# Kernel optimization log

Measured on AMD Instinct MI355X. Metric: run time of the kernel, lower is better.

## Reference

```python
import jax, jax.numpy as jnp
import numpy as np

N_NODES = 50000
N_EDGES = 500000
HIDDEN = 128
HEADS = 8
HEAD_DIM = HIDDEN // HEADS


def setup_inputs() -> dict:
    key = jax.random.key(0)
    ks = jax.random.split(key, 20)

    def lin_w(k, fin, fout):
        return (jax.random.normal(k, (fin, fout), jnp.float32) / np.sqrt(fin)).astype(jnp.float32)

    inp = {
        "h": jax.random.normal(ks[0], (N_NODES, HIDDEN), jnp.float32),
        "x": jax.random.normal(ks[1], (N_NODES, 3), jnp.float32),
        "src": jax.random.randint(ks[2], (N_EDGES,), 0, N_NODES, jnp.int32),
        "dst": jax.random.randint(ks[3], (N_EDGES,), 0, N_NODES, jnp.int32),
        "distances": jax.random.uniform(ks[4], (N_EDGES,), jnp.float32),
        # linear layers stored as [in, out] (transposed vs torch nn.Linear)
        "Wq": lin_w(ks[5], HIDDEN, HIDDEN), "bq": jnp.zeros((HIDDEN,), jnp.float32),
        "Wk": lin_w(ks[6], HIDDEN, HIDDEN), "bk": jnp.zeros((HIDDEN,), jnp.float32),
        "Wv": lin_w(ks[7], HIDDEN, HIDDEN), "bv": jnp.zeros((HIDDEN,), jnp.float32),
        "Wo": lin_w(ks[8], HIDDEN, HIDDEN), "bo": jnp.zeros((HIDDEN,), jnp.float32),
        "Wd": lin_w(ks[9], 1, HEADS), "bd": jnp.zeros((HEADS,), jnp.float32),
        "Wg1": lin_w(ks[10], HIDDEN, HIDDEN), "bg1": jnp.zeros((HIDDEN,), jnp.float32),
        "Wg2": lin_w(ks[11], HIDDEN, 1), "bg2": jnp.zeros((1,), jnp.float32),
    }
    return inp


def reference(h, x, src, dst, distances,
              Wq, bq, Wk, bk, Wv, bv, Wo, bo, Wd, bd, Wg1, bg1, Wg2, bg2):
    n = h.shape[0]
    heads = Wd.shape[1]
    dh = Wq.shape[1] // heads

    q = (h @ Wq + bq).reshape(n, heads, dh)
    k = (h @ Wk + bk).reshape(n, heads, dh)
    v = (h @ Wv + bv).reshape(n, heads, dh)

    q_src = q[src]            # [E, heads, dh]
    k_dst = k[dst]
    v_dst = v[dst]

    logits = jnp.einsum('ehd,ehd->eh', q_src, k_dst) / jnp.sqrt(jnp.asarray(dh, h.dtype))
    bias = (distances * distances)[:, None] @ Wd + bd      # [E, heads]
    lg = logits - bias

    # segment softmax over edges grouped by src node
    m = jax.ops.segment_max(lg, src, num_segments=n)        # [N, heads]
    ex = jnp.exp(lg - m[src])
    s = jax.ops.segment_sum(ex, src, num_segments=n)
    w = ex / jnp.maximum(s[src], 1e-9)                      # [E, heads]

    h_upd = jax.ops.segment_sum(v_dst * w[:, :, None], src, num_segments=n)
    h_out = h + h_upd.reshape(n, heads * dh) @ Wo + bo

    w_mean = w.mean(axis=1)                                 # mean over heads -> [E]
    disp = jax.ops.segment_sum((x[dst] - x[src]) * w_mean[:, None], src, num_segments=n)

    gate = jnp.tanh(jax.nn.silu(h_out @ Wg1 + bg1) @ Wg2 + bg2)  # [N, 1]
    x_out = x + gate * disp
    return (h_out, x_out)
```

## Files before the change

### kernel.cpp

```cpp
#include <hip/hip_runtime.h>
#include <math.h>

#define N_NODES 50000
#define N_EDGES 500000
#define HIDDEN 128
#define HEADS 8
#define HEAD_DIM 16

#define QB 391
#define QKV_TOTAL 782
#define SCAT_BLOCKS 1954
#define SPLITW_BLOCKS 320
#define ZERO_BLOCKS 196
#define NSCANB 49

typedef __attribute__((ext_vector_type(8))) short short8;
typedef __attribute__((ext_vector_type(4))) float floatx4;

#define OFF_Q       0u
#define OFF_KV      6400000u
#define OFF_HHI     12800000u
#define OFF_HLO     16000000u
#define OFF_DISP    19200000u
#define OFF_CNT     19350016u
#define OFF_ROWPTR  19400032u
#define OFF_CURSOR  19450048u
#define OFF_ESD     19500064u
#define OFF_WSPLIT  20500064u

static __device__ __forceinline__ unsigned short f2bf(float f) {
    unsigned u = __builtin_bit_cast(unsigned, f);
    unsigned r = (u + 0x7FFFu + ((u >> 16) & 1u)) >> 16;
    return (unsigned short)r;
}
static __device__ __forceinline__ float bf2f(unsigned short s) {
    return __builtin_bit_cast(float, (unsigned)s << 16);
}

__global__ void k_prep(const float* __restrict__ Wq, const float* __restrict__ Wk,
                       const float* __restrict__ Wv, const float* __restrict__ Wo,
                       const float* __restrict__ Wg1, unsigned short* __restrict__ ws,
                       int* __restrict__ cnt, int* __restrict__ flag) {
    if (blockIdx.x >= SPLITW_BLOCKS) {
        int i = (int)(blockIdx.x - SPLITW_BLOCKS) * 256 + threadIdx.x;
        if (i < N_NODES) cnt[i] = 0;
        if (i < 64) flag[i] = 0;
        return;
    }
    int t = blockIdx.x * 256 + threadIdx.x;
    int m = t >> 14, r = t & 16383;
    int k = r >> 7, n = r & 127;
    const float* W = (m == 0) ? Wq : (m == 1) ? Wk : (m == 2) ? Wv : (m == 3) ? Wo : Wg1;
    float x = W[k * 128 + n];
    int kc = k >> 5, kin = k & 31, quad = kin >> 3, j = kin & 7;
    int ct = n >> 4, nin = n & 15, lane = quad * 16 + nin;
    unsigned base = ((((unsigned)(m * 4 + kc) * 8 + ct) * 2) * 64 + lane) * 8 + j;
    unsigned short a = f2bf(x);
    ws[base] = a;
    ws[base + 512] = f2bf(x - bf2f(a));
}

__global__ void k_count(const int* __restrict__ src, int* __restrict__ cnt,
                        int* __restrict__ rnk) {
    int e = blockIdx.x * 256 + threadIdx.x;
    if (e < N_EDGES) rnk[e] = atomicAdd(&cnt[src[e]], 1);
}

__global__ __launch_bounds__(1024) void k_scan(const int* __restrict__ cnt,
                                               int* __restrict__ rowptr,
                                               int* __restrict__ agg,
                                               int* __restrict__ flag) {
    __shared__ int buf[1024];
    __shared__ int sh_off;
    const int b = blockIdx.x, t = threadIdx.x;
    const int i = b * 1024 + t;
    int val = (i < N_NODES) ? cnt[i] : 0;
    buf[t] = val;
    __syncthreads();
    for (int off = 1; off < 1024; off <<= 1) {
        int a = (t >= off) ? buf[t - off] : 0;
        __syncthreads();
        buf[t] += a;
        __syncthreads();
    }
    if (t == 1023) {
        agg[b] = buf[1023];
        __threadfence();
        atomicExch(&flag[b], 1);
    }
    if (t < 64) {
        int s = 0;
        if (t < b) {
            while (atomicAdd(&flag[t], 0) == 0) { }
            __threadfence();
            s = agg[t];
        }
#pragma unroll
        for (int off = 1; off < 64; off <<= 1) s += __shfl_xor(s, off);
        if (t == 0) sh_off = s;
    }
    __syncthreads();
    const int exoff = sh_off;
    if (i < N_NODES) rowptr[i + 1] = buf[t] + exoff;
    if (i == 0) rowptr[0] = 0;
}

__global__ __launch_bounds__(256, 2) void k_qkv_scatter(
    const float* __restrict__ h, const unsigned short* __restrict__ wsp,
    const float* __restrict__ bq, const float* __restrict__ bk, const float* __restrict__ bv,
    float* __restrict__ q, unsigned* __restrict__ kvp,
    const int* __restrict__ src, const int* __restrict__ dst,
    const float* __restrict__ dist, const int* __restrict__ rowptr,
    const int* __restrict__ rnk, int2* __restrict__ esd) {
    if (blockIdx.x >= QKV_TOTAL) {
        int e = (int)(blockIdx.x - QKV_TOTAL) * 256 + threadIdx.x;
        if (e < N_EDGES) {
            int s = src[e];
            float dd = dist[e];
            int pos = rowptr[s] + rnk[e];
            esd[pos] = make_int2(dst[e], __float_as_int(dd * dd));
        }
        return;
    }

    __shared__ short lds[32768];
    const int tid = threadIdx.x;
    const int wave = tid >> 6, lane = tid & 63;
    const int quad = lane >> 4, l15 = lane & 15;
    const bool iskv = (blockIdx.x >= QB);
    const int blk = iskv ? (int)blockIdx.x - QB : (int)blockIdx.x;
    const int row0 = blk * 128 + wave * 32;

    short8 ah[2][4], al[2][4];
#pragma unroll
    for (int rt = 0; rt < 2; ++rt) {
        int row = row0 + rt * 16 + l15;
        if (row >= N_NODES) row = N_NODES - 1;
        const float* hp = h + (size_t)row * 128;
#pragma unroll
        for (int kc = 0; kc < 4; ++kc) {
            const float* p = hp + kc * 32 + quad * 8;
            float4 f0 = *(const float4*)(p);
            float4 f1 = *(const float4*)(p + 4);
            float fv[8] = {f0.x, f0.y, f0.z, f0.w, f1.x, f1.y, f1.z, f1.w};
#pragma unroll
            for (int j = 0; j < 8; ++j) {
                unsigned short hi = f2bf(fv[j]);
                ah[rt][kc][j] = (short)hi;
                al[rt][kc][j] = (short)f2bf(fv[j] - bf2f(hi));
            }
        }
    }

    auto stage = [&](int m) {
        const float4* s4 = (const float4*)(wsp + (unsigned)m * 32768u);
        float4* d4 = (float4*)lds;
#pragma unroll 4
        for (int it = tid; it < 4096; it += 256) d4[it] = s4[it];
    };

    auto compute = [&](floatx4 (&acc)[2][8]) {
#pragma unroll
        for (int kc = 0; kc < 4; ++kc) {
#pragma unroll
            for (int ct = 0; ct < 8; ++ct) {
                const short* tb = lds + (((kc * 8 + ct) * 2) * 64 + lane) * 8;
                short8 bh = *(const short8*)(tb);
                short8 bl = *(const short8*)(tb + 512);
#pragma unroll
                for (int rt = 0; rt < 2; ++rt) {
                    acc[rt][ct] = __builtin_amdgcn_mfma_f32_16x16x32_bf16(
                        ah[rt][kc], bh, acc[rt][ct], 0, 0, 0);
                    acc[rt][ct] = __builtin_amdgcn_mfma_f32_16x16x32_bf16(
                        ah[rt][kc], bl, acc[rt][ct], 0, 0, 0);
                    acc[rt][ct] = __builtin_amdgcn_mfma_f32_16x16x32_bf16(
                        al[rt][kc], bh, acc[rt][ct], 0, 0, 0);
                }
            }
        }
    };

    if (!iskv) {
        stage(0);
        __syncthreads();
        floatx4 acc[2][8];
#pragma unroll
        for (int rt = 0; rt < 2; ++rt)
#pragma unroll
            for (int ct = 0; ct < 8; ++ct) acc[rt][ct] = (floatx4){0.f, 0.f, 0.f, 0.f};
        compute(acc);
#pragma unroll
        for (int ct = 0; ct < 8; ++ct) {
            int col = ct * 16 + l15;
            float b = bq[col];
#pragma unroll
            for (int rt = 0; rt < 2; ++rt)
#pragma unroll
                for (int reg = 0; reg < 4; ++reg) {
                    int row = row0 + rt * 16 + quad * 4 + reg;
                    if (row < N_NODES) q[(size_t)row * 128 + col] = acc[rt][ct][reg] + b;
                }
        }
    } else {
        stage(1);
        __syncthreads();
        floatx4 acc[2][8];
#pragma unroll
        for (int rt = 0; rt < 2; ++rt)
#pragma unroll
            for (int ct = 0; ct < 8; ++ct) acc[rt][ct] = (floatx4){0.f, 0.f, 0.f, 0.f};
        compute(acc);
        unsigned kb[2][8][2];
#pragma unroll
        for (int ct = 0; ct < 8; ++ct) {
            float b = bk[ct * 16 + l15];
#pragma unroll
            for (int rt = 0; rt < 2; ++rt) {
                kb[rt][ct][0] = (unsigned)f2bf(acc[rt][ct][0] + b) |
                                ((unsigned)f2bf(acc[rt][ct][1] + b) << 16);
                kb[rt][ct][1] = (unsigned)f2bf(acc[rt][ct][2] + b) |
                                ((unsigned)f2bf(acc[rt][ct][3] + b) << 16);
            }
        }
        __syncthreads();
        stage(2);
        __syncthreads();
#pragma unroll
        for (int rt = 0; rt < 2; ++rt)
#pragma unroll
            for (int ct = 0; ct < 8; ++ct) acc[rt][ct] = (floatx4){0.f, 0.f, 0.f, 0.f};
        compute(acc);
#pragma unroll
        for (int ct = 0; ct < 8; ++ct) {
            int col = ct * 16 + l15;
            float b = bv[col];
#pragma unroll
            for (int rt = 0; rt < 2; ++rt)
#pragma unroll
                for (int reg = 0; reg < 4; ++reg) {
                    int row = row0 + rt * 16 + quad * 4 + reg;
                    unsigned vb = f2bf(acc[rt][ct][reg] + b);
                    unsigned kw = (kb[rt][ct][reg >> 1] >> ((reg & 1) * 16)) & 0xFFFFu;
                    if (row < N_NODES) kvp[(size_t)row * 128 + col] = kw | (vb << 16);
                }
        }
    }
}

__global__ __launch_bounds__(256) void k_edge_node(
    const float* __restrict__ q, const unsigned* __restrict__ kvp,
    const float* __restrict__ x,
    const int2* __restrict__ esd, const int* __restrict__ rowptr,
    const float* __restrict__ Wd, const float* __restrict__ bd,
    unsigned short* __restrict__ hupd_hi, unsigned short* __restrict__ hupd_lo,
    float* __restrict__ disp) {
    const int wave = threadIdx.x >> 6, lane = threadIdx.x & 63;
    const int node = blockIdx.x * 4 + wave;
    const int h = lane >> 3, sub = lane & 7;
    const int beg = rowptr[node], end = rowptr[node + 1];

    float2 qv = *(const float2*)(q + (size_t)node * 128 + 2 * lane);
    qv.x *= 0.25f; qv.y *= 0.25f;
    const float wdh = Wd[h];
    const bool dal = (sub < 3);
    float xs = dal ? x[node * 3 + sub] : 0.f;
    const unsigned colo = 2 * lane;

    float acc0 = 0.f, acc1 = 0.f, s_own = 0.f, da = 0.f;

    for (int cb = beg; cb < end; cb += 4) {
        int2 ed[4]; uint2 kv2[4]; float xg[4]; float msk[4];
#pragma unroll
        for (int j = 0; j < 4; ++j) {
            int idx = cb + j;
            msk[j] = (idx < end) ? 1.f : 0.f;
            if (idx >= end) idx = end - 1;
            ed[j] = esd[idx];
        }
#pragma unroll
        for (int j = 0; j < 4; ++j)
            kv2[j] = *(const uint2*)(kvp + (unsigned)ed[j].x * 128u + colo);
#pragma unroll
        for (int j = 0; j < 4; ++j)
            xg[j] = dal ? x[(unsigned)ed[j].x * 3u + sub] : 0.f;
#pragma unroll
        for (int j = 0; j < 4; ++j) {
            float k0 = __builtin_bit_cast(float, kv2[j].x << 16);
            float v0 = __builtin_bit_cast(float, kv2[j].x & 0xFFFF0000u);
            float k1 = __builtin_bit_cast(float, kv2[j].y << 16);
            float v1 = __builtin_bit_cast(float, kv2[j].y & 0xFFFF0000u);
            float p = qv.x * k0 + qv.y * k1;
            p += __shfl_xor(p, 1);
            p += __shfl_xor(p, 2);
            p += __shfl_xor(p, 4);
            float w = __expf(p - __int_as_float(ed[j].y) * wdh) * msk[j];
            s_own += w;
            acc0 += v0 * w;
            acc1 += v1 * w;
            da += (xg[j] - xs) * w;
        }
    }

    float inva = 1.f / fmaxf(s_own, 1e-9f);
    float o0 = acc0 * inva, o1 = acc1 * inva;
    unsigned short h0 = f2bf(o0), h1 = f2bf(o1);
    unsigned short l0 = f2bf(o0 - bf2f(h0)), l1 = f2bf(o1 - bf2f(h1));
    ((unsigned*)hupd_hi)[(size_t)node * 64 + lane] = (unsigned)h0 | ((unsigned)h1 << 16);
    ((unsigned*)hupd_lo)[(size_t)node * 64 + lane] = (unsigned)l0 | ((unsigned)l1 << 16);

    da *= 0.125f * inva;
    da += __shfl_xor(da, 8);
    da += __shfl_xor(da, 16);
    da += __shfl_xor(da, 32);
    if (lane < 3) disp[node * 3 + lane] = da;
}

__global__ __launch_bounds__(256) void k_hout_gate(
    const float* __restrict__ h,
    const unsigned short* __restrict__ hupd_hi, const unsigned short* __restrict__ hupd_lo,
    const unsigned short* __restrict__ wsp,
    const float* __restrict__ bo, const float* __restrict__ bg1,
    const float* __restrict__ Wg2, const float* __restrict__ bg2,
    const float* __restrict__ x, const float* __restrict__ disp,
    float* __restrict__ hout, float* __restrict__ xout) {
    __shared__ float hb[4][16 * 132];
    const int wave = threadIdx.x >> 6, lane = threadIdx.x & 63;
    const int quad = lane >> 4, l15 = lane & 15;
    const int row0 = blockIdx.x * 64 + wave * 16;
    float* hbw = hb[wave];

    floatx4 acc[8];
#pragma unroll
    for (int c = 0; c < 8; ++c) acc[c] = (floatx4){0.f, 0.f, 0.f, 0.f};
#pragma unroll
    for (int kc = 0; kc < 4; ++kc) {
        int row = row0 + l15;
        if (row >= N_NODES) row = N_NODES - 1;
        size_t aoff = (size_t)row * 128 + kc * 32 + quad * 8;
        short8 ah = *(const short8*)(hupd_hi + aoff);
        short8 al = *(const short8*)(hupd_lo + aoff);
#pragma unroll
        for (int ct = 0; ct < 8; ++ct) {
            unsigned fb = ((((unsigned)(3 * 4 + kc) * 8 + ct) * 2) * 64 + lane) * 8;
            short8 bh = *(const short8*)(wsp + fb);
            short8 bl = *(const short8*)(wsp + fb + 512);
            acc[ct] = __builtin_amdgcn_mfma_f32_16x16x32_bf16(ah, bh, acc[ct], 0, 0, 0);
            acc[ct] = __builtin_amdgcn_mfma_f32_16x16x32_bf16(ah, bl, acc[ct], 0, 0, 0);
            acc[ct] = __builtin_amdgcn_mfma_f32_16x16x32_bf16(al, bh, acc[ct], 0, 0, 0);
        }
    }

#pragma unroll
    for (int ct = 0; ct < 8; ++ct) {
        int col = ct * 16 + l15;
        float bias = bo[col];
#pragma unroll
        for (int reg = 0; reg < 4; ++reg) {
            int row = row0 + quad * 4 + reg;
            float val = acc[ct][reg] + bias;
            if (row < N_NODES) {
                val += h[(size_t)row * 128 + col];
                hout[(size_t)row * 128 + col] = val;
            }
            hbw[(quad * 4 + reg) * 132 + col] = val;
        }
    }
    __asm__ volatile("s_waitcnt lgkmcnt(0)" ::: "memory");

    floatx4 acc2[8];
#pragma unroll
    for (int c = 0; c < 8; ++c) acc2[c] = (floatx4){0.f, 0.f, 0.f, 0.f};
#pragma unroll
    for (int kc = 0; kc < 4; ++kc) {
        const float* ap = hbw + l15 * 132 + kc * 32 + quad * 8;
        float4 f0 = *(const float4*)(ap);
        float4 f1 = *(const float4*)(ap + 4);
        float fv[8] = {f0.x, f0.y, f0.z, f0.w, f1.x, f1.y, f1.z, f1.w};
        short8 ah, al;
#pragma unroll
        for (int j = 0; j < 8; ++j) {
            unsigned short hi = f2bf(fv[j]);
            ah[j] = (short)hi;
            al[j] = (short)f2bf(fv[j] - bf2f(hi));
        }
#pragma unroll
        for (int ct = 0; ct < 8; ++ct) {
            unsigned fb = ((((unsigned)(4 * 4 + kc) * 8 + ct) * 2) * 64 + lane) * 8;
            short8 bh = *(const short8*)(wsp + fb);
            short8 bl = *(const short8*)(wsp + fb + 512);
            acc2[ct] = __builtin_amdgcn_mfma_f32_16x16x32_bf16(ah, bh, acc2[ct], 0, 0, 0);
            acc2[ct] = __builtin_amdgcn_mfma_f32_16x16x32_bf16(ah, bl, acc2[ct], 0, 0, 0);
            acc2[ct] = __builtin_amdgcn_mfma_f32_16x16x32_bf16(al, bh, acc2[ct], 0, 0, 0);
        }
    }

    float pr[4] = {0.f, 0.f, 0.f, 0.f};
#pragma unroll
    for (int ct = 0; ct < 8; ++ct) {
        int col = ct * 16 + l15;
        float b1 = bg1[col];
        float w2 = Wg2[col];
#pragma unroll
        for (int reg = 0; reg < 4; ++reg) {
            float z = acc2[ct][reg] + b1;
            pr[reg] += (z / (1.f + __expf(-z))) * w2;
        }
    }
#pragma unroll
    for (int off = 1; off < 16; off <<= 1) {
#pragma unroll
        for (int reg = 0; reg < 4; ++reg) pr[reg] += __shfl_xor(pr[reg], off);
    }
    if (l15 == 0) {
        float b2 = bg2[0];
#pragma unroll
        for (int reg = 0; reg < 4; ++reg) {
            int row = row0 + quad * 4 + reg;
            if (row < N_NODES) {
                float g = tanhf(pr[reg] + b2);
#pragma unroll
                for (int dd = 0; dd < 3; ++dd) {
                    int oo = row * 3 + dd;
                    xout[oo] = x[oo] + g * disp[oo];
                }
            }
        }
    }
}

extern "C" void kernel_launch(void* const* d_in, const int* in_sizes, int n_in,
                              void* d_out, int out_size, void* d_ws, size_t ws_size,
                              hipStream_t stream) {
    const float* h    = (const float*)d_in[0];
    const float* x    = (const float*)d_in[1];
    const int*   src  = (const int*)d_in[2];
    const int*   dst  = (const int*)d_in[3];
    const float* dist = (const float*)d_in[4];
    const float* Wq = (const float*)d_in[5];  const float* bq = (const float*)d_in[6];
    const float* Wk = (const float*)d_in[7];  const float* bk = (const float*)d_in[8];
    const float* Wv = (const float*)d_in[9];  const float* bv = (const float*)d_in[10];
    const float* Wo = (const float*)d_in[11]; const float* bo = (const float*)d_in[12];
    const float* Wd = (const float*)d_in[13]; const float* bd = (const float*)d_in[14];
    const float* Wg1 = (const float*)d_in[15]; const float* bg1 = (const float*)d_in[16];
    const float* Wg2 = (const float*)d_in[17]; const float* bg2 = (const float*)d_in[18];

    float* ws    = (float*)d_ws;
    float* q     = ws + OFF_Q;
    unsigned* kvp = (unsigned*)(ws + OFF_KV);
    float* disp  = ws + OFF_DISP;
    int* cnt     = (int*)(ws + OFF_CNT);
    int* rowptr  = (int*)(ws + OFF_ROWPTR);
    int* agg     = (int*)(ws + OFF_CURSOR);
    int* flag    = agg + 64;
    int2* esd    = (int2*)(ws + OFF_ESD);
    unsigned short* wsp = (unsigned short*)(ws + OFF_WSPLIT);
    int* rank   = (int*)(ws + OFF_HHI);
    unsigned short* hupd_hi = (unsigned short*)(ws + OFF_HHI);
    unsigned short* hupd_lo = (unsigned short*)(ws + OFF_HLO);
    float* hout = (float*)d_out;
    float* xout = hout + (size_t)N_NODES * HIDDEN;

    k_prep<<<SPLITW_BLOCKS + ZERO_BLOCKS, 256, 0, stream>>>(Wq, Wk, Wv, Wo, Wg1, wsp,
                                                            cnt, flag);
    k_count<<<SCAT_BLOCKS, 256, 0, stream>>>(src, cnt, rank);
    k_scan<<<NSCANB, 1024, 0, stream>>>(cnt, rowptr, agg, flag);
    k_qkv_scatter<<<QKV_TOTAL + SCAT_BLOCKS, 256, 0, stream>>>(
        h, wsp, bq, bk, bv, q, kvp, src, dst, dist, rowptr, rank, esd);
    k_edge_node<<<N_NODES / 4, 256, 0, stream>>>(q, kvp, x, esd, rowptr,
                                                 Wd, bd, hupd_hi, hupd_lo, disp);
    k_hout_gate<<<(N_NODES + 63) / 64, 256, 0, stream>>>(h, hupd_hi, hupd_lo, wsp,
                                                         bo, bg1, Wg2, bg2,
                                                         x, disp, hout, xout);
}
```

Measured before the change: 265.4 us.

## Batch edge-index loads via wave shuffles and double row tiles in hout/gate GEMM

```diff
diff --git a/kernel.cpp b/kernel.cpp
--- a/kernel.cpp
+++ b/kernel.cpp
@@ -13,6 +13,7 @@
 #define SPLITW_BLOCKS 320
 #define ZERO_BLOCKS 196
 #define NSCANB 49
+#define HG_BLOCKS 391
 
 typedef __attribute__((ext_vector_type(8))) short short8;
 typedef __attribute__((ext_vector_type(4))) float floatx4;
@@ -268,36 +269,64 @@
 
     float acc0 = 0.f, acc1 = 0.f, s_own = 0.f, da = 0.f;
 
-    for (int cb = beg; cb < end; cb += 4) {
-        int2 ed[4]; uint2 kv2[4]; float xg[4]; float msk[4];
-#pragma unroll
-        for (int j = 0; j < 4; ++j) {
-            int idx = cb + j;
-            msk[j] = (idx < end) ? 1.f : 0.f;
-            if (idx >= end) idx = end - 1;
-            ed[j] = esd[idx];
-        }
-#pragma unroll
-        for (int j = 0; j < 4; ++j)
-            kv2[j] = *(const uint2*)(kvp + (unsigned)ed[j].x * 128u + colo);
-#pragma unroll
-        for (int j = 0; j < 4; ++j)
-            xg[j] = dal ? x[(unsigned)ed[j].x * 3u + sub] : 0.f;
-#pragma unroll
-        for (int j = 0; j < 4; ++j) {
-            float k0 = __builtin_bit_cast(float, kv2[j].x << 16);
-            float v0 = __builtin_bit_cast(float, kv2[j].x & 0xFFFF0000u);
-            float k1 = __builtin_bit_cast(float, kv2[j].y << 16);
-            float v1 = __builtin_bit_cast(float, kv2[j].y & 0xFFFF0000u);
+    for (int cb = beg; cb < end; cb += 64) {
+        int idx = cb + lane;
+        int dvec = 0; float d2vec = 0.f;
+        if (idx < end) {
+            int2 ed = esd[idx];
+            dvec = ed.x;
+            d2vec = __int_as_float(ed.y);
+        }
+        int clen = min(64, end - cb);
+        int i = 0;
+        for (; i + 4 <= clen; i += 4) {
+            int di[4]; float dd2[4]; uint2 kv2[4]; float xg[4];
+#pragma unroll
+            for (int j = 0; j < 4; ++j) {
+                di[j]  = __shfl(dvec, i + j);
+                dd2[j] = __shfl(d2vec, i + j);
+            }
+#pragma unroll
+            for (int j = 0; j < 4; ++j)
+                kv2[j] = *(const uint2*)(kvp + (unsigned)di[j] * 128u + colo);
+#pragma unroll
+            for (int j = 0; j < 4; ++j)
+                xg[j] = dal ? x[(unsigned)di[j] * 3u + sub] : 0.f;
+#pragma unroll
+            for (int j = 0; j < 4; ++j) {
+                float k0 = __builtin_bit_cast(float, kv2[j].x << 16);
+                float v0 = __builtin_bit_cast(float, kv2[j].x & 0xFFFF0000u);
+                float k1 = __builtin_bit_cast(float, kv2[j].y << 16);
+                float v1 = __builtin_bit_cast(float, kv2[j].y & 0xFFFF0000u);
+                float p = qv.x * k0 + qv.y * k1;
+                p += __shfl_xor(p, 1);
+                p += __shfl_xor(p, 2);
+                p += __shfl_xor(p, 4);
+                float w = __expf(p - dd2[j] * wdh);
+                s_own += w;
+                acc0 += v0 * w;
+                acc1 += v1 * w;
+                da += (xg[j] - xs) * w;
+            }
+        }
+        for (; i < clen; ++i) {
+            int dij  = __shfl(dvec, i);
+            float d2 = __shfl(d2vec, i);
+            uint2 kv2 = *(const uint2*)(kvp + (unsigned)dij * 128u + colo);
+            float xgj = dal ? x[(unsigned)dij * 3u + sub] : 0.f;
+            float k0 = __builtin_bit_cast(float, kv2.x << 16);
+            float v0 = __builtin_bit_cast(float, kv2.x & 0xFFFF0000u);
+            float k1 = __builtin_bit_cast(float, kv2.y << 16);
+            float v1 = __builtin_bit_cast(float, kv2.y & 0xFFFF0000u);
             float p = qv.x * k0 + qv.y * k1;
             p += __shfl_xor(p, 1);
             p += __shfl_xor(p, 2);
             p += __shfl_xor(p, 4);
-            float w = __expf(p - __int_as_float(ed[j].y) * wdh) * msk[j];
+            float w = __expf(p - d2 * wdh);
             s_own += w;
             acc0 += v0 * w;
             acc1 += v1 * w;
-            da += (xg[j] - xs) * w;
+            da += (xgj - xs) * w;
         }
     }
 
@@ -315,7 +344,7 @@
     if (lane < 3) disp[node * 3 + lane] = da;
 }
 
-__global__ __launch_bounds__(256) void k_hout_gate(
+__global__ __launch_bounds__(256, 2) void k_hout_gate(
     const float* __restrict__ h,
     const unsigned short* __restrict__ hupd_hi, const unsigned short* __restrict__ hupd_lo,
     const unsigned short* __restrict__ wsp,
@@ -323,30 +352,39 @@
     const float* __restrict__ Wg2, const float* __restrict__ bg2,
     const float* __restrict__ x, const float* __restrict__ disp,
     float* __restrict__ hout, float* __restrict__ xout) {
-    __shared__ float hb[4][16 * 132];
+    __shared__ float hb[4][32 * 132];
     const int wave = threadIdx.x >> 6, lane = threadIdx.x & 63;
     const int quad = lane >> 4, l15 = lane & 15;
-    const int row0 = blockIdx.x * 64 + wave * 16;
+    const int row0 = blockIdx.x * 128 + wave * 32;
     float* hbw = hb[wave];
 
-    floatx4 acc[8];
-#pragma unroll
-    for (int c = 0; c < 8; ++c) acc[c] = (floatx4){0.f, 0.f, 0.f, 0.f};
+    floatx4 acc[2][8];
+#pragma unroll
+    for (int rt = 0; rt < 2; ++rt)
+#pragma unroll
+        for (int c = 0; c < 8; ++c) acc[rt][c] = (floatx4){0.f, 0.f, 0.f, 0.f};
 #pragma unroll
     for (int kc = 0; kc < 4; ++kc) {
-        int row = row0 + l15;
-        if (row >= N_NODES) row = N_NODES - 1;
-        size_t aoff = (size_t)row * 128 + kc * 32 + quad * 8;
-        short8 ah = *(const short8*)(hupd_hi + aoff);
-        short8 al = *(const short8*)(hupd_lo + aoff);
+        short8 ah[2], al[2];
+#pragma unroll
+        for (int rt = 0; rt < 2; ++rt) {
+            int row = row0 + rt * 16 + l15;
+            if (row >= N_NODES) row = N_NODES - 1;
+            size_t aoff = (size_t)row * 128 + kc * 32 + quad * 8;
+            ah[rt] = *(const short8*)(hupd_hi + aoff);
+            al[rt] = *(const short8*)(hupd_lo + aoff);
+        }
 #pragma unroll
         for (int ct = 0; ct < 8; ++ct) {
             unsigned fb = ((((unsigned)(3 * 4 + kc) * 8 + ct) * 2) * 64 + lane) * 8;
             short8 bh = *(const short8*)(wsp + fb);
             short8 bl = *(const short8*)(wsp + fb + 512);
-            acc[ct] = __builtin_amdgcn_mfma_f32_16x16x32_bf16(ah, bh, acc[ct], 0, 0, 0);
-            acc[ct] = __builtin_amdgcn_mfma_f32_16x16x32_bf16(ah, bl, acc[ct], 0, 0, 0);
-            acc[ct] = __builtin_amdgcn_mfma_f32_16x16x32_bf16(al, bh, acc[ct], 0, 0, 0);
+#pragma unroll
+            for (int rt = 0; rt < 2; ++rt) {
+                acc[rt][ct] = __builtin_amdgcn_mfma_f32_16x16x32_bf16(ah[rt], bh, acc[rt][ct], 0, 0, 0);
+                acc[rt][ct] = __builtin_amdgcn_mfma_f32_16x16x32_bf16(ah[rt], bl, acc[rt][ct], 0, 0, 0);
+                acc[rt][ct] = __builtin_amdgcn_mfma_f32_16x16x32_bf16(al[rt], bh, acc[rt][ct], 0, 0, 0);
+            }
         }
     }
 
@@ -355,76 +393,93 @@
         int col = ct * 16 + l15;
         float bias = bo[col];
 #pragma unroll
-        for (int reg = 0; reg < 4; ++reg) {
-            int row = row0 + quad * 4 + reg;
-            float val = acc[ct][reg] + bias;
-            if (row < N_NODES) {
-                val += h[(size_t)row * 128 + col];
-                hout[(size_t)row * 128 + col] = val;
-            }
-            hbw[(quad * 4 + reg) * 132 + col] = val;
-        }
+        for (int rt = 0; rt < 2; ++rt)
+#pragma unroll
+            for (int reg = 0; reg < 4; ++reg) {
+                int lrow = rt * 16 + quad * 4 + reg;
+                int row = row0 + lrow;
+                float val = acc[rt][ct][reg] + bias;
+                if (row < N_NODES) {
+                    val += h[(size_t)row * 128 + col];
+                    hout[(size_t)row * 128 + col] = val;
+                }
+                hbw[lrow * 132 + col] = val;
+            }
     }
     __asm__ volatile("s_waitcnt lgkmcnt(0)" ::: "memory");
 
-    floatx4 acc2[8];
-#pragma unroll
-    for (int c = 0; c < 8; ++c) acc2[c] = (floatx4){0.f, 0.f, 0.f, 0.f};
+    floatx4 acc2[2][8];
+#pragma unroll
+    for (int rt = 0; rt < 2; ++rt)
+#pragma unroll
+        for (int c = 0; c < 8; ++c) acc2[rt][c] = (floatx4){0.f, 0.f, 0.f, 0.f};
 #pragma unroll
     for (int kc = 0; kc < 4; ++kc) {
-        const float* ap = hbw + l15 * 132 + kc * 32 + quad * 8;
-        float4 f0 = *(const float4*)(ap);
-        float4 f1 = *(const float4*)(ap + 4);
-        float fv[8] = {f0.x, f0.y, f0.z, f0.w, f1.x, f1.y, f1.z, f1.w};
-        short8 ah, al;
-#pragma unroll
-        for (int j = 0; j < 8; ++j) {
-            unsigned short hi = f2bf(fv[j]);
-            ah[j] = (short)hi;
-            al[j] = (short)f2bf(fv[j] - bf2f(hi));
+        short8 a2h[2], a2l[2];
+#pragma unroll
+        for (int rt = 0; rt < 2; ++rt) {
+            const float* ap = hbw + (rt * 16 + l15) * 132 + kc * 32 + quad * 8;
+            float4 f0 = *(const float4*)(ap);
+            float4 f1 = *(const float4*)(ap + 4);
+            float fv[8] = {f0.x, f0.y, f0.z, f0.w, f1.x, f1.y, f1.z, f1.w};
+#pragma unroll
+            for (int j = 0; j < 8; ++j) {
+                unsigned short hi = f2bf(fv[j]);
+                a2h[rt][j] = (short)hi;
+                a2l[rt][j] = (short)f2bf(fv[j] - bf2f(hi));
+            }
         }
 #pragma unroll
         for (int ct = 0; ct < 8; ++ct) {
             unsigned fb = ((((unsigned)(4 * 4 + kc) * 8 + ct) * 2) * 64 + lane) * 8;
             short8 bh = *(const short8*)(wsp + fb);
             short8 bl = *(const short8*)(wsp + fb + 512);
-            acc2[ct] = __builtin_amdgcn_mfma_f32_16x16x32_bf16(ah, bh, acc2[ct], 0, 0, 0);
-            acc2[ct] = __builtin_amdgcn_mfma_f32_16x16x32_bf16(ah, bl, acc2[ct], 0, 0, 0);
-            acc2[ct] = __builtin_amdgcn_mfma_f32_16x16x32_bf16(al, bh, acc2[ct], 0, 0, 0);
-        }
-    }
-
-    float pr[4] = {0.f, 0.f, 0.f, 0.f};
+#pragma unroll
+            for (int rt = 0; rt < 2; ++rt) {
+                acc2[rt][ct] = __builtin_amdgcn_mfma_f32_16x16x32_bf16(a2h[rt], bh, acc2[rt][ct], 0, 0, 0);
+                acc2[rt][ct] = __builtin_amdgcn_mfma_f32_16x16x32_bf16(a2h[rt], bl, acc2[rt][ct], 0, 0, 0);
+                acc2[rt][ct] = __builtin_amdgcn_mfma_f32_16x16x32_bf16(a2l[rt], bh, acc2[rt][ct], 0, 0, 0);
+            }
+        }
+    }
+
+    float pr[2][4] = {{0.f, 0.f, 0.f, 0.f}, {0.f, 0.f, 0.f, 0.f}};
 #pragma unroll
     for (int ct = 0; ct < 8; ++ct) {
         int col = ct * 16 + l15;
         float b1 = bg1[col];
         float w2 = Wg2[col];
 #pragma unroll
-        for (int reg = 0; reg < 4; ++reg) {
-            float z = acc2[ct][reg] + b1;
-            pr[reg] += (z / (1.f + __expf(-z))) * w2;
-        }
+        for (int rt = 0; rt < 2; ++rt)
+#pragma unroll
+            for (int reg = 0; reg < 4; ++reg) {
+                float z = acc2[rt][ct][reg] + b1;
+                pr[rt][reg] += (z / (1.f + __expf(-z))) * w2;
+            }
     }
 #pragma unroll
     for (int off = 1; off < 16; off <<= 1) {
 #pragma unroll
-        for (int reg = 0; reg < 4; ++reg) pr[reg] += __shfl_xor(pr[reg], off);
+        for (int rt = 0; rt < 2; ++rt)
+#pragma unroll
+            for (int reg = 0; reg < 4; ++reg) pr[rt][reg] += __shfl_xor(pr[rt][reg], off);
     }
     if (l15 == 0) {
         float b2 = bg2[0];
 #pragma unroll
-        for (int reg = 0; reg < 4; ++reg) {
-            int row = row0 + quad * 4 + reg;
-            if (row < N_NODES) {
-                float g = tanhf(pr[reg] + b2);
-#pragma unroll
-                for (int dd = 0; dd < 3; ++dd) {
-                    int oo = row * 3 + dd;
-                    xout[oo] = x[oo] + g * disp[oo];
+        for (int rt = 0; rt < 2; ++rt)
+#pragma unroll
+            for (int reg = 0; reg < 4; ++reg) {
+                int row = row0 + rt * 16 + quad * 4 + reg;
+                if (row < N_NODES) {
+                    float g = tanhf(pr[rt][reg] + b2);
+#pragma unroll
+                    for (int dd = 0; dd < 3; ++dd) {
+                        int oo = row * 3 + dd;
+                        xout[oo] = x[oo] + g * disp[oo];
+                    }
                 }
             }
-        }
     }
 }
 
@@ -468,7 +523,7 @@
         h, wsp, bq, bk, bv, q, kvp, src, dst, dist, rowptr, rank, esd);
     k_edge_node<<<N_NODES / 4, 256, 0, stream>>>(q, kvp, x, esd, rowptr,
                                                  Wd, bd, hupd_hi, hupd_lo, disp);
-    k_hout_gate<<<(N_NODES + 63) / 64, 256, 0, stream>>>(h, hupd_hi, hupd_lo, wsp,
-                                                         bo, bg1, Wg2, bg2,
-                                                         x, disp, hout, xout);
-}
+    k_hout_gate<<<HG_BLOCKS, 256, 0, stream>>>(h, hupd_hi, hupd_lo, wsp,
+                                               bo, bg1, Wg2, bg2,
+                                               x, disp, hout, xout);
+}
```

Result: no change. 267.8 us (+0.9%).

## Cooperatively load edge lists per wave and enlarge QKV blocks to 512 threads

Applied to the files above, without the earlier changes.

```diff
diff --git a/kernel.cpp b/kernel.cpp
--- a/kernel.cpp
+++ b/kernel.cpp
@@ -7,9 +7,10 @@
 #define HEADS 8
 #define HEAD_DIM 16
 
-#define QB 391
-#define QKV_TOTAL 782
-#define SCAT_BLOCKS 1954
+#define QB 196
+#define QKV_TOTAL 392
+#define SCAT_BLOCKS 977
+#define CNT_BLOCKS 1954
 #define SPLITW_BLOCKS 320
 #define ZERO_BLOCKS 196
 #define NSCANB 49
@@ -105,7 +106,7 @@
     if (i == 0) rowptr[0] = 0;
 }
 
-__global__ __launch_bounds__(256, 2) void k_qkv_scatter(
+__global__ __launch_bounds__(512, 4) void k_qkv_scatter(
     const float* __restrict__ h, const unsigned short* __restrict__ wsp,
     const float* __restrict__ bq, const float* __restrict__ bk, const float* __restrict__ bv,
     float* __restrict__ q, unsigned* __restrict__ kvp,
@@ -113,7 +114,7 @@
     const float* __restrict__ dist, const int* __restrict__ rowptr,
     const int* __restrict__ rnk, int2* __restrict__ esd) {
     if (blockIdx.x >= QKV_TOTAL) {
-        int e = (int)(blockIdx.x - QKV_TOTAL) * 256 + threadIdx.x;
+        int e = (int)(blockIdx.x - QKV_TOTAL) * 512 + threadIdx.x;
         if (e < N_EDGES) {
             int s = src[e];
             float dd = dist[e];
@@ -129,7 +130,7 @@
     const int quad = lane >> 4, l15 = lane & 15;
     const bool iskv = (blockIdx.x >= QB);
     const int blk = iskv ? (int)blockIdx.x - QB : (int)blockIdx.x;
-    const int row0 = blk * 128 + wave * 32;
+    const int row0 = blk * 256 + wave * 32;
 
     short8 ah[2][4], al[2][4];
 #pragma unroll
@@ -156,7 +157,7 @@
         const float4* s4 = (const float4*)(wsp + (unsigned)m * 32768u);
         float4* d4 = (float4*)lds;
 #pragma unroll 4
-        for (int it = tid; it < 4096; it += 256) d4[it] = s4[it];
+        for (int it = tid; it < 4096; it += 512) d4[it] = s4[it];
     };
 
     auto compute = [&](floatx4 (&acc)[2][8]) {
@@ -268,36 +269,64 @@
 
     float acc0 = 0.f, acc1 = 0.f, s_own = 0.f, da = 0.f;
 
-    for (int cb = beg; cb < end; cb += 4) {
-        int2 ed[4]; uint2 kv2[4]; float xg[4]; float msk[4];
-#pragma unroll
-        for (int j = 0; j < 4; ++j) {
-            int idx = cb + j;
-            msk[j] = (idx < end) ? 1.f : 0.f;
-            if (idx >= end) idx = end - 1;
-            ed[j] = esd[idx];
-        }
-#pragma unroll
-        for (int j = 0; j < 4; ++j)
-            kv2[j] = *(const uint2*)(kvp + (unsigned)ed[j].x * 128u + colo);
-#pragma unroll
-        for (int j = 0; j < 4; ++j)
-            xg[j] = dal ? x[(unsigned)ed[j].x * 3u + sub] : 0.f;
-#pragma unroll
-        for (int j = 0; j < 4; ++j) {
-            float k0 = __builtin_bit_cast(float, kv2[j].x << 16);
-            float v0 = __builtin_bit_cast(float, kv2[j].x & 0xFFFF0000u);
-            float k1 = __builtin_bit_cast(float, kv2[j].y << 16);
-            float v1 = __builtin_bit_cast(float, kv2[j].y & 0xFFFF0000u);
+    for (int cb = beg; cb < end; cb += 64) {
+        int idx = cb + lane;
+        int dvec = 0; float d2vec = 0.f;
+        if (idx < end) {
+            int2 ed = esd[idx];
+            dvec = ed.x;
+            d2vec = __int_as_float(ed.y);
+        }
+        int clen = min(64, end - cb);
+        int i = 0;
+        for (; i + 4 <= clen; i += 4) {
+            int di[4]; float dd2[4]; uint2 kv2[4]; float xg[4];
+#pragma unroll
+            for (int j = 0; j < 4; ++j) {
+                di[j]  = __shfl(dvec, i + j);
+                dd2[j] = __shfl(d2vec, i + j);
+            }
+#pragma unroll
+            for (int j = 0; j < 4; ++j)
+                kv2[j] = *(const uint2*)(kvp + (unsigned)di[j] * 128u + colo);
+#pragma unroll
+            for (int j = 0; j < 4; ++j)
+                xg[j] = dal ? x[(unsigned)di[j] * 3u + sub] : 0.f;
+#pragma unroll
+            for (int j = 0; j < 4; ++j) {
+                float k0 = __builtin_bit_cast(float, kv2[j].x << 16);
+                float v0 = __builtin_bit_cast(float, kv2[j].x & 0xFFFF0000u);
+                float k1 = __builtin_bit_cast(float, kv2[j].y << 16);
+                float v1 = __builtin_bit_cast(float, kv2[j].y & 0xFFFF0000u);
+                float p = qv.x * k0 + qv.y * k1;
+                p += __shfl_xor(p, 1);
+                p += __shfl_xor(p, 2);
+                p += __shfl_xor(p, 4);
+                float w = __expf(p - dd2[j] * wdh);
+                s_own += w;
+                acc0 += v0 * w;
+                acc1 += v1 * w;
+                da += (xg[j] - xs) * w;
+            }
+        }
+        for (; i < clen; ++i) {
+            int dij  = __shfl(dvec, i);
+            float d2 = __shfl(d2vec, i);
+            uint2 kv2 = *(const uint2*)(kvp + (unsigned)dij * 128u + colo);
+            float xgj = dal ? x[(unsigned)dij * 3u + sub] : 0.f;
+            float k0 = __builtin_bit_cast(float, kv2.x << 16);
+            float v0 = __builtin_bit_cast(float, kv2.x & 0xFFFF0000u);
+            float k1 = __builtin_bit_cast(float, kv2.y << 16);
+            float v1 = __builtin_bit_cast(float, kv2.y & 0xFFFF0000u);
             float p = qv.x * k0 + qv.y * k1;
             p += __shfl_xor(p, 1);
             p += __shfl_xor(p, 2);
             p += __shfl_xor(p, 4);
-            float w = __expf(p - __int_as_float(ed[j].y) * wdh) * msk[j];
+            float w = __expf(p - d2 * wdh);
             s_own += w;
             acc0 += v0 * w;
             acc1 += v1 * w;
-            da += (xg[j] - xs) * w;
+            da += (xgj - xs) * w;
         }
     }
 
@@ -462,9 +491,9 @@
 
     k_prep<<<SPLITW_BLOCKS + ZERO_BLOCKS, 256, 0, stream>>>(Wq, Wk, Wv, Wo, Wg1, wsp,
                                                             cnt, flag);
-    k_count<<<SCAT_BLOCKS, 256, 0, stream>>>(src, cnt, rank);
+    k_count<<<CNT_BLOCKS, 256, 0, stream>>>(src, cnt, rank);
     k_scan<<<NSCANB, 1024, 0, stream>>>(cnt, rowptr, agg, flag);
-    k_qkv_scatter<<<QKV_TOTAL + SCAT_BLOCKS, 256, 0, stream>>>(
+    k_qkv_scatter<<<QKV_TOTAL + SCAT_BLOCKS, 512, 0, stream>>>(
         h, wsp, bq, bk, bv, q, kvp, src, dst, dist, rowptr, rank, esd);
     k_edge_node<<<N_NODES / 4, 256, 0, stream>>>(q, kvp, x, esd, rowptr,
                                                  Wd, bd, hupd_hi, hupd_lo, disp);
```

New measurement: 286.9 us. 1.08x slower.
